# Kernel optimization log

Measured on AMD Instinct MI355X. Metric: run time of the kernel, lower is better.

Reference implementation:

```python
import jax, jax.numpy as jnp
import numpy as np

B, N, IN_F, OUT_F, REL_DIM, NUM_REL = 4, 2048, 256, 128, 10, 6
D = OUT_F // 2  # internal_dim
ALPHA = 0.2
LAMBDA_INIT = 0.8 - 0.6 * float(np.exp(-0.3 * 1))  # depth=1
EPS = 1e-5


def setup_inputs() -> dict:
    key = jax.random.key(0)
    ks = jax.random.split(key, 16)
    return {
        "h": jax.random.normal(ks[0], (B, N, IN_F), jnp.float32),
        "adj": jax.random.randint(ks[1], (B, N, N), 0, NUM_REL, jnp.int32),
        "W": jax.random.normal(ks[2], (IN_F, OUT_F), jnp.float32) * (1.414 / np.sqrt(IN_F)),
        "a_left_pos": jax.random.normal(ks[3], (D,), jnp.float32) * 0.1,
        "a_right_pos": jax.random.normal(ks[4], (D,), jnp.float32) * 0.1,
        "a_left_neg": jax.random.normal(ks[5], (D,), jnp.float32) * 0.1,
        "a_right_neg": jax.random.normal(ks[6], (D,), jnp.float32) * 0.1,
        "rel_emb": jax.random.normal(ks[7], (NUM_REL, REL_DIM), jnp.float32),
        "a_rel_pos": jax.random.normal(ks[8], (REL_DIM,), jnp.float32) * 0.3,
        "a_rel_neg": jax.random.normal(ks[9], (REL_DIM,), jnp.float32) * 0.3,
        "lambda_left1": jax.random.normal(ks[10], (D,), jnp.float32) * 0.1,
        "lambda_right1": jax.random.normal(ks[11], (D,), jnp.float32) * 0.1,
        "lambda_left2": jax.random.normal(ks[12], (D,), jnp.float32) * 0.1,
        "lambda_right2": jax.random.normal(ks[13], (D,), jnp.float32) * 0.1,
        "ln_gamma": jnp.ones((OUT_F,), jnp.float32),
        "ln_beta": jnp.zeros((OUT_F,), jnp.float32),
    }


def _leaky_relu(x):
    return jnp.where(x >= 0, x, ALPHA * x)


def reference(h, adj, W, a_left_pos, a_right_pos, a_left_neg, a_right_neg,
              rel_emb, a_rel_pos, a_rel_neg,
              lambda_left1, lambda_right1, lambda_left2, lambda_right2,
              ln_gamma, ln_beta):
    Wh = jnp.einsum('bnf,fo->bno', h, W)              # [B,N,OUT_F]
    Wh4 = Wh.reshape(B, N, 2, D)
    Wh_pos, Wh_neg = Wh4[:, :, 0, :], Wh4[:, :, 1, :]  # [B,N,D]

    # e[b,i,j] = left[b,i] + right[b,j] + rel_score[adj[b,i,j]]
    # relation Linear(rel_dim,1) applied to embedding rows == per-relation scalar lookup
    rel_score_pos = rel_emb @ a_rel_pos               # [NUM_REL]
    rel_score_neg = rel_emb @ a_rel_neg
    e_pos = (Wh_pos @ a_left_pos)[:, :, None] + (Wh_pos @ a_right_pos)[:, None, :] + rel_score_pos[adj]
    e_neg = (Wh_neg @ a_left_neg)[:, :, None] + (Wh_neg @ a_right_neg)[:, None, :] + rel_score_neg[adj]

    neg_inf = jnp.float32(-9e15)
    mask = adj > 0
    attn_pos = jax.nn.softmax(jnp.where(mask, _leaky_relu(e_pos), neg_inf), axis=2)
    attn_neg = jax.nn.softmax(jnp.where(mask, _leaky_relu(e_neg), neg_inf), axis=2)

    lam1 = jnp.exp(jnp.sum(lambda_left1 * lambda_right1))
    lam2 = jnp.exp(jnp.sum(lambda_left2 * lambda_right2))
    lambda_full = lam1 - lam2 + LAMBDA_INIT
    attention = attn_pos - lambda_full * attn_neg     # [B,N,N]

    Wh_v = jnp.concatenate([Wh_pos, Wh_neg], axis=-1)  # [B,N,OUT_F]
    h_prime = jnp.einsum('bij,bjo->bio', attention, Wh_v)

    mu = jnp.mean(h_prime, axis=-1, keepdims=True)
    var = jnp.mean(jnp.square(h_prime - mu), axis=-1, keepdims=True)
    h_prime = (h_prime - mu) * jax.lax.rsqrt(var + EPS) * ln_gamma + ln_beta
    h_prime = h_prime * (1.0 - LAMBDA_INIT)
    return jax.nn.gelu(h_prime, approximate=False), attention
```

## Files before the change

kernel.cpp:

```cpp
#include <hip/hip_runtime.h>
#include <math.h>

typedef short bf16x8 __attribute__((ext_vector_type(8)));
typedef float f32x4  __attribute__((ext_vector_type(4)));

constexpr int   B_    = 4;
constexpr int   N_    = 2048;
constexpr int   INF_  = 256;
constexpr int   OUTF_ = 128;
constexpr float LAMBDA_INIT_ = 0.35550906759096926f;
constexpr float OUT_SCALE_   = 0.64449093240903074f;
constexpr float EPS_         = 1e-5f;
constexpr float LOG2E_       = 1.44269504088896340736f;

__device__ inline unsigned short f2bf(float x) {
  unsigned u = __float_as_uint(x);
  u += 0x7fffu + ((u >> 16) & 1u);
  return (unsigned short)(u >> 16);
}
__device__ inline unsigned pack2(float a, float b) {
  return (unsigned)f2bf(a) | ((unsigned)f2bf(b) << 16);
}

__global__ void scalars_kernel(const float* __restrict__ rel_emb,
                               const float* __restrict__ a_rel_pos,
                               const float* __restrict__ a_rel_neg,
                               const float* __restrict__ ll1, const float* __restrict__ lr1,
                               const float* __restrict__ ll2, const float* __restrict__ lr2,
                               float* __restrict__ scal) {
  int lane = threadIdx.x;
  float p1 = ll1[lane] * lr1[lane];
  float p2 = ll2[lane] * lr2[lane];
  #pragma unroll
  for (int off = 32; off; off >>= 1) { p1 += __shfl_xor(p1, off); p2 += __shfl_xor(p2, off); }
  if (lane == 0) scal[12] = expf(p1) - expf(p2) + LAMBDA_INIT_;
  if (lane < 6) {
    float sp = 0.f, sn = 0.f;
    for (int k = 0; k < 10; ++k) {
      float rv = rel_emb[lane * 10 + k];
      sp += rv * a_rel_pos[k];
      sn += rv * a_rel_neg[k];
    }
    scal[lane]     = sp * LOG2E_;
    scal[6 + lane] = sn * LOG2E_;
  }
}

__global__ __launch_bounds__(256) void wh_kernel(const float* __restrict__ h,
                                                 const float* __restrict__ W,
                                                 float* __restrict__ Wh,
                                                 unsigned short* __restrict__ WhvT) {
  __shared__ __align__(16) float hT[INF_][20];
  const int t = threadIdx.x;
  const size_t row0 = (size_t)blockIdx.x * 16;
  #pragma unroll
  for (int i = 0; i < 16; ++i) hT[t][i] = h[(row0 + i) * INF_ + t];
  __syncthreads();
  const int c  = t & 127;
  const int rg = t >> 7;
  float acc[8] = {0.f, 0.f, 0.f, 0.f, 0.f, 0.f, 0.f, 0.f};
  #pragma unroll 4
  for (int k = 0; k < INF_; ++k) {
    float wv = W[k * OUTF_ + c];
    const float4* hp = reinterpret_cast<const float4*>(&hT[k][rg * 8]);
    float4 h0 = hp[0], h1 = hp[1];
    acc[0] += h0.x * wv; acc[1] += h0.y * wv; acc[2] += h0.z * wv; acc[3] += h0.w * wv;
    acc[4] += h1.x * wv; acc[5] += h1.y * wv; acc[6] += h1.z * wv; acc[7] += h1.w * wv;
  }
  #pragma unroll
  for (int r = 0; r < 8; ++r) Wh[(row0 + rg * 8 + r) * OUTF_ + c] = acc[r];
  uint4 pk;
  pk.x = pack2(acc[0], acc[1]); pk.y = pack2(acc[2], acc[3]);
  pk.z = pack2(acc[4], acc[5]); pk.w = pack2(acc[6], acc[7]);
  const int b  = (int)(row0 >> 11);
  const int n0 = (int)(row0 & 2047) + rg * 8;
  *reinterpret_cast<uint4*>(WhvT + ((size_t)b * OUTF_ + c) * N_ + n0) = pk;
}

__global__ __launch_bounds__(256) void dots_kernel(const float* __restrict__ Wh,
                                                   const float* __restrict__ alp, const float* __restrict__ arp,
                                                   const float* __restrict__ aln, const float* __restrict__ arn,
                                                   float* __restrict__ lposv, float* __restrict__ rposv,
                                                   float* __restrict__ lnegv, float* __restrict__ rnegv) {
  const int t = threadIdx.x;
  const int wid = t >> 6, lane = t & 63;
  const int node = blockIdx.x * 4 + wid;
  float wp = Wh[(size_t)node * OUTF_ + lane];
  float wn = Wh[(size_t)node * OUTF_ + 64 + lane];
  float s0 = wp * alp[lane], s1 = wp * arp[lane];
  float s2 = wn * aln[lane], s3 = wn * arn[lane];
  #pragma unroll
  for (int off = 32; off; off >>= 1) {
    s0 += __shfl_xor(s0, off); s1 += __shfl_xor(s1, off);
    s2 += __shfl_xor(s2, off); s3 += __shfl_xor(s3, off);
  }
  if (lane == 0) {
    lposv[node] = s0 * LOG2E_; rposv[node] = s1 * LOG2E_;
    lnegv[node] = s2 * LOG2E_; rnegv[node] = s3 * LOG2E_;
  }
}

__global__ __launch_bounds__(512) void attn_v3b(
    const int* __restrict__ adj,
    const float* __restrict__ lposv, const float* __restrict__ rposv,
    const float* __restrict__ lnegv, const float* __restrict__ rnegv,
    const float* __restrict__ scal, float* __restrict__ out1,
    unsigned short* __restrict__ abf, int writeAbf) {
  __shared__ float sums[16];
  const int t = threadIdx.x;
  const int lane = t & 63;
  const int wv = t >> 6;
  const int flat = blockIdx.x;
  const int b = flat >> 11;

  const float lam = scal[12];
  float srcP = -1.0e30f, srcN = -1.0e30f;
  if (lane >= 1 && lane <= 5) { srcP = scal[lane]; srcN = scal[6 + lane]; }
  const int iSrcP = __float_as_int(srcP);
  const int iSrcN = __float_as_int(srcN);

  const float lP = lposv[flat];
  const float lN = lnegv[flat];
  const int j0 = t * 4;
  int4   av4 = *reinterpret_cast<const int4*>(adj + (size_t)flat * N_ + j0);
  float4 rp4 = *reinterpret_cast<const float4*>(rposv + b * N_ + j0);
  float4 rn4 = *reinterpret_cast<const float4*>(rnegv + b * N_ + j0);
  int   av[4] = {av4.x, av4.y, av4.z, av4.w};
  float rp[4] = {rp4.x, rp4.y, rp4.z, rp4.w};
  float rn[4] = {rn4.x, rn4.y, rn4.z, rn4.w};

  float p[4], n[4];
  #pragma unroll
  for (int q = 0; q < 4; ++q) {
    float rsp = __int_as_float(__builtin_amdgcn_ds_bpermute(av[q] << 2, iSrcP));
    float rsn = __int_as_float(__builtin_amdgcn_ds_bpermute(av[q] << 2, iSrcN));
    float e  = lP + rp[q] + rsp;
    float en = lN + rn[q] + rsn;
    e  = fmaxf(e, 0.2f * e);
    en = fmaxf(en, 0.2f * en);
    p[q] = __builtin_amdgcn_exp2f(e);
    n[q] = __builtin_amdgcn_exp2f(en);
  }
  float sP = (p[0] + p[1]) + (p[2] + p[3]);
  float sN = (n[0] + n[1]) + (n[2] + n[3]);
  #pragma unroll
  for (int off = 32; off; off >>= 1) { sP += __shfl_xor(sP, off); sN += __shfl_xor(sN, off); }
  if (lane == 0) { sums[wv] = sP; sums[8 + wv] = sN; }
  __syncthreads();
  const float sPT = ((sums[0] + sums[1]) + (sums[2] + sums[3])) +
                    ((sums[4] + sums[5]) + (sums[6] + sums[7]));
  const float sNT = ((sums[8] + sums[9]) + (sums[10] + sums[11])) +
                    ((sums[12] + sums[13]) + (sums[14] + sums[15]));
  const float s1 = 1.f / sPT;
  const float s2 = -lam / sNT;

  float a[4];
  #pragma unroll
  for (int q = 0; q < 4; ++q) a[q] = p[q] * s1 + n[q] * s2;
  float* o1 = out1 + (size_t)flat * N_ + j0;
  *reinterpret_cast<float4*>(o1) = make_float4(a[0], a[1], a[2], a[3]);
  if (writeAbf) {
    uint2 u;
    u.x = pack2(a[0], a[1]); u.y = pack2(a[2], a[3]);
    *reinterpret_cast<uint2*>(abf + (size_t)flat * N_ + j0) = u;
  }
}

__global__ __launch_bounds__(512) void pv_v5(
    const float* __restrict__ attn, const unsigned short* __restrict__ abf, int useAbf,
    const unsigned short* __restrict__ WhvT,
    const float* __restrict__ gamma, const float* __restrict__ beta,
    float* __restrict__ out0) {
  __shared__ __align__(16) uint4 A4[2][16 * 32];
  __shared__ __align__(16) float hp[16][132];
  const int t = threadIdx.x;
  const int lane = t & 63;
  const int w = t >> 6;
  const int bi = blockIdx.x;
  const int b  = bi >> 7;
  const int i0 = (bi & 127) * 16;

  const int sr = t >> 5;
  const int sj = t & 31;
  const float4* src4 = reinterpret_cast<const float4*>(
      attn + ((size_t)(b * N_ + i0 + sr)) * N_ + sj * 8);
  const uint4* srcU = reinterpret_cast<const uint4*>(
      abf + ((size_t)(b * N_ + i0 + sr)) * N_) + sj;
  const int swz = sr & 7;
  const int ui = sr * 32 + (sj ^ swz);

  const int bl  = lane & 15;
  const int kg  = lane >> 4;
  const int ch  = w * 16 + bl;
  const unsigned short* Bp = WhvT + ((size_t)b * OUTF_ + ch) * N_ + kg * 8;
  f32x4 acc0 = {0.f, 0.f, 0.f, 0.f};
  f32x4 acc1 = {0.f, 0.f, 0.f, 0.f};
  const int arow = bl * 32;
  const int aswz = bl & 7;

  if (useAbf) {
    A4[0][ui] = srcU[0];
  } else {
    float4 s0 = src4[0], s1 = src4[1];
    uint4 u;
    u.x = pack2(s0.x, s0.y); u.y = pack2(s0.z, s0.w);
    u.z = pack2(s1.x, s1.y); u.w = pack2(s1.z, s1.w);
    A4[0][ui] = u;
  }
  __syncthreads();

  for (int c = 0; c < 8; ++c) {
    const int cur = c & 1;
    float4 s0, s1;
    uint4 t0;
    if (c < 7) {
      if (useAbf) {
        t0 = srcU[(c + 1) * 32];
      } else {
        const int o = (c + 1) * 64;
        s0 = src4[o]; s1 = src4[o + 1];
      }
    }
    const unsigned short* bp = Bp + c * 256;
    #pragma unroll
    for (int kk = 0; kk < 8; ++kk) {
      bf16x8 a  = *reinterpret_cast<const bf16x8*>(&A4[cur][arow + ((kk * 4 + kg) ^ aswz)]);
      bf16x8 bv = *reinterpret_cast<const bf16x8*>(bp + kk * 32);
      if (cur == 0) acc0 = __builtin_amdgcn_mfma_f32_16x16x32_bf16(a, bv, acc0, 0, 0, 0);
      else          acc1 = __builtin_amdgcn_mfma_f32_16x16x32_bf16(a, bv, acc1, 0, 0, 0);
    }
    if (c < 7) {
      if (useAbf) {
        A4[cur ^ 1][ui] = t0;
      } else {
        uint4 u;
        u.x = pack2(s0.x, s0.y); u.y = pack2(s0.z, s0.w);
        u.z = pack2(s1.x, s1.y); u.w = pack2(s1.z, s1.w);
        A4[cur ^ 1][ui] = u;
      }
    }
    __syncthreads();
  }

  #pragma unroll
  for (int q = 0; q < 4; ++q) hp[kg * 4 + q][ch] = acc0[q] + acc1[q];
  __syncthreads();

  const int row = t >> 5;
  const int c0  = t & 31;
  float v[4], s = 0.f, sq = 0.f;
  #pragma unroll
  for (int e = 0; e < 4; ++e) {
    v[e] = hp[row][c0 + e * 32];
    s += v[e]; sq += v[e] * v[e];
  }
  #pragma unroll
  for (int off = 16; off; off >>= 1) { s += __shfl_xor(s, off); sq += __shfl_xor(sq, off); }
  const float mu  = s  * (1.f / 128.f);
  const float var = sq * (1.f / 128.f) - mu * mu;
  const float inv = rsqrtf(var + EPS_);
  float* orow = out0 + ((size_t)(b * N_ + i0 + row)) * OUTF_;
  #pragma unroll
  for (int e = 0; e < 4; ++e) {
    const int chh = c0 + e * 32;
    float y = (v[e] - mu) * inv * gamma[chh] + beta[chh];
    y *= OUT_SCALE_;
    orow[chh] = 0.5f * y * (1.f + erff(y * 0.70710678118654752f));
  }
}

extern "C" void kernel_launch(void* const* d_in, const int* in_sizes, int n_in,
                              void* d_out, int out_size, void* d_ws, size_t ws_size,
                              hipStream_t stream) {
  (void)in_sizes; (void)n_in; (void)out_size;
  const float* h        = (const float*)d_in[0];
  const int*   adj      = (const int*)d_in[1];
  const float* W        = (const float*)d_in[2];
  const float* alp      = (const float*)d_in[3];
  const float* arp      = (const float*)d_in[4];
  const float* aln      = (const float*)d_in[5];
  const float* arn      = (const float*)d_in[6];
  const float* rel_emb  = (const float*)d_in[7];
  const float* a_rel_p  = (const float*)d_in[8];
  const float* a_rel_n  = (const float*)d_in[9];
  const float* ll1      = (const float*)d_in[10];
  const float* lr1      = (const float*)d_in[11];
  const float* ll2      = (const float*)d_in[12];
  const float* lr2      = (const float*)d_in[13];
  const float* gamma    = (const float*)d_in[14];
  const float* beta     = (const float*)d_in[15];

  float* out0 = (float*)d_out;
  float* out1 = out0 + (size_t)B_ * N_ * OUTF_;

  float* ws    = (float*)d_ws;
  float* scal  = ws;
  float* lposv = ws + 32;
  float* rposv = lposv + B_ * N_;
  float* lnegv = rposv + B_ * N_;
  float* rnegv = lnegv + B_ * N_;
  float* Wh    = rnegv + B_ * N_;
  unsigned short* WhvT = (unsigned short*)(Wh + (size_t)B_ * N_ * OUTF_);
  unsigned short* Abf  = WhvT + (size_t)B_ * N_ * OUTF_;

  const size_t need = (size_t)(32 + 4 * B_ * N_ + B_ * N_ * OUTF_) * 4
                    + (size_t)B_ * N_ * OUTF_ * 2
                    + (size_t)B_ * N_ * N_ * 2;
  const int useAbf = (ws_size >= need) ? 1 : 0;

  scalars_kernel<<<1, 64, 0, stream>>>(rel_emb, a_rel_p, a_rel_n, ll1, lr1, ll2, lr2, scal);
  wh_kernel<<<(B_ * N_) / 16, 256, 0, stream>>>(h, W, Wh, WhvT);
  dots_kernel<<<(B_ * N_) / 4, 256, 0, stream>>>(Wh, alp, arp, aln, arn, lposv, rposv, lnegv, rnegv);
  attn_v3b<<<B_ * N_, 512, 0, stream>>>(adj, lposv, rposv, lnegv, rnegv, scal, out1, Abf, useAbf);
  pv_v5<<<B_ * (N_ / 16), 512, 0, stream>>>(out1, Abf, useAbf, WhvT, gamma, beta, out0);
}
```

Baseline: 97.18 us.

## Split PV reduction across two wave groups and shuffle-reduce softmax sums

The PV kernel now runs 1024 threads per block. Two groups of eight waves each take alternate K chunks into separate accumulators, and the two partial results are summed in shared memory before the LayerNorm/GELU epilogue. This halves the serial K-loop length per wave and loads two chunks per stage, which should raise latency hiding for the 512-block grid. In the attention kernel, the final cross-wave sum is now a lane-parallel shuffle reduction instead of every thread reading all 16 shared values. The costs are more shared memory, an extra partial-sum pass, and half the threads sitting idle in the epilogue.

Result: no change. 98.23 us (+1.1%).

```diff
diff --git a/kernel.cpp b/kernel.cpp
--- a/kernel.cpp
+++ b/kernel.cpp
@@ -100,7 +100,7 @@
   }
 }
 
-__global__ __launch_bounds__(512) void attn_v3b(
+__global__ __launch_bounds__(512) void attn_v3c(
     const int* __restrict__ adj,
     const float* __restrict__ lposv, const float* __restrict__ rposv,
     const float* __restrict__ lnegv, const float* __restrict__ rnegv,
@@ -147,12 +147,12 @@
   for (int off = 32; off; off >>= 1) { sP += __shfl_xor(sP, off); sN += __shfl_xor(sN, off); }
   if (lane == 0) { sums[wv] = sP; sums[8 + wv] = sN; }
   __syncthreads();
-  const float sPT = ((sums[0] + sums[1]) + (sums[2] + sums[3])) +
-                    ((sums[4] + sums[5]) + (sums[6] + sums[7]));
-  const float sNT = ((sums[8] + sums[9]) + (sums[10] + sums[11])) +
-                    ((sums[12] + sums[13]) + (sums[14] + sums[15]));
-  const float s1 = 1.f / sPT;
-  const float s2 = -lam / sNT;
+  float vP = sums[lane & 7];
+  vP += __shfl_xor(vP, 1); vP += __shfl_xor(vP, 2); vP += __shfl_xor(vP, 4);
+  float vN = sums[8 + (lane & 7)];
+  vN += __shfl_xor(vN, 1); vN += __shfl_xor(vN, 2); vN += __shfl_xor(vN, 4);
+  const float s1 = 1.f / vP;
+  const float s2 = -lam / vN;
 
   float a[4];
   #pragma unroll
@@ -166,13 +166,13 @@
   }
 }
 
-__global__ __launch_bounds__(512) void pv_v5(
+__global__ __launch_bounds__(1024, 8) void pv_v6(
     const float* __restrict__ attn, const unsigned short* __restrict__ abf, int useAbf,
     const unsigned short* __restrict__ WhvT,
     const float* __restrict__ gamma, const float* __restrict__ beta,
     float* __restrict__ out0) {
-  __shared__ __align__(16) uint4 A4[2][16 * 32];
-  __shared__ __align__(16) float hp[16][132];
+  __shared__ __align__(16) uint4 A4[2][2][512];
+  __shared__ __align__(16) float hp2[2][16][132];
   const int t = threadIdx.x;
   const int lane = t & 63;
   const int w = t >> 6;
@@ -180,92 +180,93 @@
   const int b  = bi >> 7;
   const int i0 = (bi & 127) * 16;
 
-  const int sr = t >> 5;
-  const int sj = t & 31;
-  const float4* src4 = reinterpret_cast<const float4*>(
-      attn + ((size_t)(b * N_ + i0 + sr)) * N_ + sj * 8);
+  const int sr = t >> 6;
+  const int sj = t & 63;
+  const int sbuf = sj >> 5;
+  const int su   = sj & 31;
+  const int swz  = sr & 7;
+  const int slot = sr * 32 + (su ^ swz);
   const uint4* srcU = reinterpret_cast<const uint4*>(
       abf + ((size_t)(b * N_ + i0 + sr)) * N_) + sj;
-  const int swz = sr & 7;
-  const int ui = sr * 32 + (sj ^ swz);
-
+  const float4* src4 = reinterpret_cast<const float4*>(
+      attn + ((size_t)(b * N_ + i0 + sr)) * N_) + sj * 2;
+
+  const int cw  = w >> 3;
   const int bl  = lane & 15;
   const int kg  = lane >> 4;
-  const int ch  = w * 16 + bl;
+  const int ch  = (w & 7) * 16 + bl;
   const unsigned short* Bp = WhvT + ((size_t)b * OUTF_ + ch) * N_ + kg * 8;
-  f32x4 acc0 = {0.f, 0.f, 0.f, 0.f};
-  f32x4 acc1 = {0.f, 0.f, 0.f, 0.f};
+  f32x4 acc = {0.f, 0.f, 0.f, 0.f};
   const int arow = bl * 32;
   const int aswz = bl & 7;
 
   if (useAbf) {
-    A4[0][ui] = srcU[0];
+    A4[0][sbuf][slot] = srcU[0];
   } else {
     float4 s0 = src4[0], s1 = src4[1];
     uint4 u;
     u.x = pack2(s0.x, s0.y); u.y = pack2(s0.z, s0.w);
     u.z = pack2(s1.x, s1.y); u.w = pack2(s1.z, s1.w);
-    A4[0][ui] = u;
+    A4[0][sbuf][slot] = u;
   }
   __syncthreads();
 
-  for (int c = 0; c < 8; ++c) {
-    const int cur = c & 1;
+  for (int pi = 0; pi < 4; ++pi) {
+    const int pb = pi & 1;
     float4 s0, s1;
     uint4 t0;
-    if (c < 7) {
-      if (useAbf) {
-        t0 = srcU[(c + 1) * 32];
-      } else {
-        const int o = (c + 1) * 64;
-        s0 = src4[o]; s1 = src4[o + 1];
-      }
-    }
+    if (pi < 3) {
+      if (useAbf) t0 = srcU[(pi + 1) * 64];
+      else { s0 = src4[(pi + 1) * 128]; s1 = src4[(pi + 1) * 128 + 1]; }
+    }
+    const int c = 2 * pi + cw;
     const unsigned short* bp = Bp + c * 256;
     #pragma unroll
     for (int kk = 0; kk < 8; ++kk) {
-      bf16x8 a  = *reinterpret_cast<const bf16x8*>(&A4[cur][arow + ((kk * 4 + kg) ^ aswz)]);
+      bf16x8 a  = *reinterpret_cast<const bf16x8*>(&A4[pb][cw][arow + ((kk * 4 + kg) ^ aswz)]);
       bf16x8 bv = *reinterpret_cast<const bf16x8*>(bp + kk * 32);
-      if (cur == 0) acc0 = __builtin_amdgcn_mfma_f32_16x16x32_bf16(a, bv, acc0, 0, 0, 0);
-      else          acc1 = __builtin_amdgcn_mfma_f32_16x16x32_bf16(a, bv, acc1, 0, 0, 0);
-    }
-    if (c < 7) {
+      acc = __builtin_amdgcn_mfma_f32_16x16x32_bf16(a, bv, acc, 0, 0, 0);
+    }
+    if (pi < 3) {
       if (useAbf) {
-        A4[cur ^ 1][ui] = t0;
+        A4[pb ^ 1][sbuf][slot] = t0;
       } else {
         uint4 u;
         u.x = pack2(s0.x, s0.y); u.y = pack2(s0.z, s0.w);
         u.z = pack2(s1.x, s1.y); u.w = pack2(s1.z, s1.w);
-        A4[cur ^ 1][ui] = u;
+        A4[pb ^ 1][sbuf][slot] = u;
       }
     }
     __syncthreads();
   }
 
   #pragma unroll
-  for (int q = 0; q < 4; ++q) hp[kg * 4 + q][ch] = acc0[q] + acc1[q];
+  for (int q = 0; q < 4; ++q) hp2[cw][kg * 4 + q][ch] = acc[q];
   __syncthreads();
 
-  const int row = t >> 5;
-  const int c0  = t & 31;
-  float v[4], s = 0.f, sq = 0.f;
-  #pragma unroll
-  for (int e = 0; e < 4; ++e) {
-    v[e] = hp[row][c0 + e * 32];
-    s += v[e]; sq += v[e] * v[e];
-  }
-  #pragma unroll
-  for (int off = 16; off; off >>= 1) { s += __shfl_xor(s, off); sq += __shfl_xor(sq, off); }
-  const float mu  = s  * (1.f / 128.f);
-  const float var = sq * (1.f / 128.f) - mu * mu;
-  const float inv = rsqrtf(var + EPS_);
-  float* orow = out0 + ((size_t)(b * N_ + i0 + row)) * OUTF_;
-  #pragma unroll
-  for (int e = 0; e < 4; ++e) {
-    const int chh = c0 + e * 32;
-    float y = (v[e] - mu) * inv * gamma[chh] + beta[chh];
-    y *= OUT_SCALE_;
-    orow[chh] = 0.5f * y * (1.f + erff(y * 0.70710678118654752f));
+  if (t < 512) {
+    const int row = t >> 5;
+    const int c0  = t & 31;
+    float v[4], s = 0.f, sq = 0.f;
+    #pragma unroll
+    for (int e = 0; e < 4; ++e) {
+      const int chh = c0 + e * 32;
+      v[e] = hp2[0][row][chh] + hp2[1][row][chh];
+      s += v[e]; sq += v[e] * v[e];
+    }
+    #pragma unroll
+    for (int off = 16; off; off >>= 1) { s += __shfl_xor(s, off); sq += __shfl_xor(sq, off); }
+    const float mu  = s  * (1.f / 128.f);
+    const float var = sq * (1.f / 128.f) - mu * mu;
+    const float inv = rsqrtf(var + EPS_);
+    float* orow = out0 + ((size_t)(b * N_ + i0 + row)) * OUTF_;
+    #pragma unroll
+    for (int e = 0; e < 4; ++e) {
+      const int chh = c0 + e * 32;
+      float y = (v[e] - mu) * inv * gamma[chh] + beta[chh];
+      y *= OUT_SCALE_;
+      orow[chh] = 0.5f * y * (1.f + erff(y * 0.70710678118654752f));
+    }
   }
 }
 
@@ -311,6 +312,6 @@
   scalars_kernel<<<1, 64, 0, stream>>>(rel_emb, a_rel_p, a_rel_n, ll1, lr1, ll2, lr2, scal);
   wh_kernel<<<(B_ * N_) / 16, 256, 0, stream>>>(h, W, Wh, WhvT);
   dots_kernel<<<(B_ * N_) / 4, 256, 0, stream>>>(Wh, alp, arp, aln, arn, lposv, rposv, lnegv, rnegv);
-  attn_v3b<<<B_ * N_, 512, 0, stream>>>(adj, lposv, rposv, lnegv, rnegv, scal, out1, Abf, useAbf);
-  pv_v5<<<B_ * (N_ / 16), 512, 0, stream>>>(out1, Abf, useAbf, WhvT, gamma, beta, out0);
-}
+  attn_v3c<<<B_ * N_, 512, 0, stream>>>(adj, lposv, rposv, lnegv, rnegv, scal, out1, Abf, useAbf);
+  pv_v6<<<B_ * (N_ / 16), 1024, 0, stream>>>(out1, Abf, useAbf, WhvT, gamma, beta, out0);
+}
```

## Fuse attention-logit dot products into Wh GEMM and drop the bf16 attention copy

Applied to the files above, without the earlier changes.

Folds the left/right attention dot products into the Wh projection kernel, using wave shuffles on the accumulators, which removes one launch and a re-read of Wh. The attention kernel no longer writes a separate bf16 copy of the attention matrix. The PV kernel now always reads the fp32 attention output and packs it to bf16 itself, trading a 32 MB extra write and 32 MB read for a larger fp32 read. The block-sum reduction is also switched from a serial LDS read chain to shuffles.

Result: faster. 91.30 us (-6.1%).

```diff
diff --git a/kernel.cpp b/kernel.cpp
--- a/kernel.cpp
+++ b/kernel.cpp
@@ -46,10 +46,13 @@
   }
 }
 
-__global__ __launch_bounds__(256) void wh_kernel(const float* __restrict__ h,
-                                                 const float* __restrict__ W,
-                                                 float* __restrict__ Wh,
-                                                 unsigned short* __restrict__ WhvT) {
+__global__ __launch_bounds__(256) void wh_dots_kernel(
+    const float* __restrict__ h, const float* __restrict__ W,
+    const float* __restrict__ alp, const float* __restrict__ arp,
+    const float* __restrict__ aln, const float* __restrict__ arn,
+    float* __restrict__ Wh, unsigned short* __restrict__ WhvT,
+    float* __restrict__ lposv, float* __restrict__ rposv,
+    float* __restrict__ lnegv, float* __restrict__ rnegv) {
   __shared__ __align__(16) float hT[INF_][20];
   const int t = threadIdx.x;
   const size_t row0 = (size_t)blockIdx.x * 16;
@@ -75,37 +78,38 @@
   const int b  = (int)(row0 >> 11);
   const int n0 = (int)(row0 & 2047) + rg * 8;
   *reinterpret_cast<uint4*>(WhvT + ((size_t)b * OUTF_ + c) * N_ + n0) = pk;
-}
-
-__global__ __launch_bounds__(256) void dots_kernel(const float* __restrict__ Wh,
-                                                   const float* __restrict__ alp, const float* __restrict__ arp,
-                                                   const float* __restrict__ aln, const float* __restrict__ arn,
-                                                   float* __restrict__ lposv, float* __restrict__ rposv,
-                                                   float* __restrict__ lnegv, float* __restrict__ rnegv) {
-  const int t = threadIdx.x;
-  const int wid = t >> 6, lane = t & 63;
-  const int node = blockIdx.x * 4 + wid;
-  float wp = Wh[(size_t)node * OUTF_ + lane];
-  float wn = Wh[(size_t)node * OUTF_ + 64 + lane];
-  float s0 = wp * alp[lane], s1 = wp * arp[lane];
-  float s2 = wn * aln[lane], s3 = wn * arn[lane];
+
+  const int lane = t & 63;
+  const int wv   = t >> 6;
+  const bool pos = (wv & 1) == 0;
+  const float al = pos ? alp[lane] : aln[lane];
+  const float ar = pos ? arp[lane] : arn[lane];
+  float sl[8], sr2[8];
+  #pragma unroll
+  for (int r = 0; r < 8; ++r) { sl[r] = acc[r] * al; sr2[r] = acc[r] * ar; }
   #pragma unroll
   for (int off = 32; off; off >>= 1) {
-    s0 += __shfl_xor(s0, off); s1 += __shfl_xor(s1, off);
-    s2 += __shfl_xor(s2, off); s3 += __shfl_xor(s3, off);
+    #pragma unroll
+    for (int r = 0; r < 8; ++r) {
+      sl[r]  += __shfl_xor(sl[r],  off);
+      sr2[r] += __shfl_xor(sr2[r], off);
+    }
   }
   if (lane == 0) {
-    lposv[node] = s0 * LOG2E_; rposv[node] = s1 * LOG2E_;
-    lnegv[node] = s2 * LOG2E_; rnegv[node] = s3 * LOG2E_;
-  }
-}
-
-__global__ __launch_bounds__(512) void attn_v3b(
+    #pragma unroll
+    for (int r = 0; r < 8; ++r) {
+      const int node = (int)row0 + rg * 8 + r;
+      if (pos) { lposv[node] = sl[r] * LOG2E_; rposv[node] = sr2[r] * LOG2E_; }
+      else     { lnegv[node] = sl[r] * LOG2E_; rnegv[node] = sr2[r] * LOG2E_; }
+    }
+  }
+}
+
+__global__ __launch_bounds__(512) void attn_v3d(
     const int* __restrict__ adj,
     const float* __restrict__ lposv, const float* __restrict__ rposv,
     const float* __restrict__ lnegv, const float* __restrict__ rnegv,
-    const float* __restrict__ scal, float* __restrict__ out1,
-    unsigned short* __restrict__ abf, int writeAbf) {
+    const float* __restrict__ scal, float* __restrict__ out1) {
   __shared__ float sums[16];
   const int t = threadIdx.x;
   const int lane = t & 63;
@@ -147,28 +151,22 @@
   for (int off = 32; off; off >>= 1) { sP += __shfl_xor(sP, off); sN += __shfl_xor(sN, off); }
   if (lane == 0) { sums[wv] = sP; sums[8 + wv] = sN; }
   __syncthreads();
-  const float sPT = ((sums[0] + sums[1]) + (sums[2] + sums[3])) +
-                    ((sums[4] + sums[5]) + (sums[6] + sums[7]));
-  const float sNT = ((sums[8] + sums[9]) + (sums[10] + sums[11])) +
-                    ((sums[12] + sums[13]) + (sums[14] + sums[15]));
-  const float s1 = 1.f / sPT;
-  const float s2 = -lam / sNT;
+  float vP = sums[lane & 7];
+  vP += __shfl_xor(vP, 1); vP += __shfl_xor(vP, 2); vP += __shfl_xor(vP, 4);
+  float vN = sums[8 + (lane & 7)];
+  vN += __shfl_xor(vN, 1); vN += __shfl_xor(vN, 2); vN += __shfl_xor(vN, 4);
+  const float s1 = 1.f / vP;
+  const float s2 = -lam / vN;
 
   float a[4];
   #pragma unroll
   for (int q = 0; q < 4; ++q) a[q] = p[q] * s1 + n[q] * s2;
   float* o1 = out1 + (size_t)flat * N_ + j0;
   *reinterpret_cast<float4*>(o1) = make_float4(a[0], a[1], a[2], a[3]);
-  if (writeAbf) {
-    uint2 u;
-    u.x = pack2(a[0], a[1]); u.y = pack2(a[2], a[3]);
-    *reinterpret_cast<uint2*>(abf + (size_t)flat * N_ + j0) = u;
-  }
-}
-
-__global__ __launch_bounds__(512) void pv_v5(
-    const float* __restrict__ attn, const unsigned short* __restrict__ abf, int useAbf,
-    const unsigned short* __restrict__ WhvT,
+}
+
+__global__ __launch_bounds__(512) void pv_v5b(
+    const float* __restrict__ attn, const unsigned short* __restrict__ WhvT,
     const float* __restrict__ gamma, const float* __restrict__ beta,
     float* __restrict__ out0) {
   __shared__ __align__(16) uint4 A4[2][16 * 32];
@@ -184,8 +182,6 @@
   const int sj = t & 31;
   const float4* src4 = reinterpret_cast<const float4*>(
       attn + ((size_t)(b * N_ + i0 + sr)) * N_ + sj * 8);
-  const uint4* srcU = reinterpret_cast<const uint4*>(
-      abf + ((size_t)(b * N_ + i0 + sr)) * N_) + sj;
   const int swz = sr & 7;
   const int ui = sr * 32 + (sj ^ swz);
 
@@ -198,9 +194,7 @@
   const int arow = bl * 32;
   const int aswz = bl & 7;
 
-  if (useAbf) {
-    A4[0][ui] = srcU[0];
-  } else {
+  {
     float4 s0 = src4[0], s1 = src4[1];
     uint4 u;
     u.x = pack2(s0.x, s0.y); u.y = pack2(s0.z, s0.w);
@@ -212,14 +206,9 @@
   for (int c = 0; c < 8; ++c) {
     const int cur = c & 1;
     float4 s0, s1;
-    uint4 t0;
     if (c < 7) {
-      if (useAbf) {
-        t0 = srcU[(c + 1) * 32];
-      } else {
-        const int o = (c + 1) * 64;
-        s0 = src4[o]; s1 = src4[o + 1];
-      }
+      const int o = (c + 1) * 64;
+      s0 = src4[o]; s1 = src4[o + 1];
     }
     const unsigned short* bp = Bp + c * 256;
     #pragma unroll
@@ -230,14 +219,10 @@
       else          acc1 = __builtin_amdgcn_mfma_f32_16x16x32_bf16(a, bv, acc1, 0, 0, 0);
     }
     if (c < 7) {
-      if (useAbf) {
-        A4[cur ^ 1][ui] = t0;
-      } else {
-        uint4 u;
-        u.x = pack2(s0.x, s0.y); u.y = pack2(s0.z, s0.w);
-        u.z = pack2(s1.x, s1.y); u.w = pack2(s1.z, s1.w);
-        A4[cur ^ 1][ui] = u;
-      }
+      uint4 u;
+      u.x = pack2(s0.x, s0.y); u.y = pack2(s0.z, s0.w);
+      u.z = pack2(s1.x, s1.y); u.w = pack2(s1.z, s1.w);
+      A4[cur ^ 1][ui] = u;
     }
     __syncthreads();
   }
@@ -272,7 +257,7 @@
 extern "C" void kernel_launch(void* const* d_in, const int* in_sizes, int n_in,
                               void* d_out, int out_size, void* d_ws, size_t ws_size,
                               hipStream_t stream) {
-  (void)in_sizes; (void)n_in; (void)out_size;
+  (void)in_sizes; (void)n_in; (void)out_size; (void)ws_size;
   const float* h        = (const float*)d_in[0];
   const int*   adj      = (const int*)d_in[1];
   const float* W        = (const float*)d_in[2];
@@ -301,16 +286,10 @@
   float* rnegv = lnegv + B_ * N_;
   float* Wh    = rnegv + B_ * N_;
   unsigned short* WhvT = (unsigned short*)(Wh + (size_t)B_ * N_ * OUTF_);
-  unsigned short* Abf  = WhvT + (size_t)B_ * N_ * OUTF_;
-
-  const size_t need = (size_t)(32 + 4 * B_ * N_ + B_ * N_ * OUTF_) * 4
-                    + (size_t)B_ * N_ * OUTF_ * 2
-                    + (size_t)B_ * N_ * N_ * 2;
-  const int useAbf = (ws_size >= need) ? 1 : 0;
 
   scalars_kernel<<<1, 64, 0, stream>>>(rel_emb, a_rel_p, a_rel_n, ll1, lr1, ll2, lr2, scal);
-  wh_kernel<<<(B_ * N_) / 16, 256, 0, stream>>>(h, W, Wh, WhvT);
-  dots_kernel<<<(B_ * N_) / 4, 256, 0, stream>>>(Wh, alp, arp, aln, arn, lposv, rposv, lnegv, rnegv);
-  attn_v3b<<<B_ * N_, 512, 0, stream>>>(adj, lposv, rposv, lnegv, rnegv, scal, out1, Abf, useAbf);
-  pv_v5<<<B_ * (N_ / 16), 512, 0, stream>>>(out1, Abf, useAbf, WhvT, gamma, beta, out0);
-}
+  wh_dots_kernel<<<(B_ * N_) / 16, 256, 0, stream>>>(h, W, alp, arp, aln, arn,
+                                                     Wh, WhvT, lposv, rposv, lnegv, rnegv);
+  attn_v3d<<<B_ * N_, 512, 0, stream>>>(adj, lposv, rposv, lnegv, rnegv, scal, out1);
+  pv_v5b<<<B_ * (N_ / 16), 512, 0, stream>>>(out1, WhvT, gamma, beta, out0);
+}
```
